# Kernel tuning notes

Measured on AMD Instinct MI355X. Metric: run time of the kernel, lower is better.

## Reference

```python
import jax, jax.numpy as jnp
import numpy as np

BS = 32  # leaf block size


def setup_inputs() -> dict:
    key = jax.random.key(0)
    ks = jax.random.split(key, 10)
    N, C, E, H = 262144, 128, 4194304, 4
    x = jax.random.normal(ks[0], (1, N, C), jnp.float32)
    rows = jax.random.randint(ks[1], (E,), 0, N, dtype=jnp.int32)
    offs = jax.random.randint(ks[2], (E,), -16, 16, dtype=jnp.int32)
    cols = jnp.clip(rows + offs, 0, N - 1)
    edge_index = jnp.stack([rows, cols], axis=0)  # (2, E) int32
    edge_values = jax.random.normal(ks[3], (E,), jnp.float32)
    positions = jax.random.uniform(ks[4], (N, 3), jnp.float32)
    qkv_w = jax.random.normal(ks[5], (C, 3 * C), jnp.float32) * 0.02
    qkv_b = jnp.zeros((3 * C,), jnp.float32)
    proj_w = jax.random.normal(ks[6], (C, C), jnp.float32) * 0.02
    proj_b = jnp.zeros((C,), jnp.float32)
    gate_w = jax.random.normal(ks[7], (H, 1), jnp.float32) * 0.01  # nn.Linear(1, H)
    gate_b = jnp.zeros((H,), jnp.float32)
    return {"x": x, "edge_index": edge_index, "edge_values": edge_values,
            "positions": positions, "qkv_w": qkv_w, "qkv_b": qkv_b,
            "proj_w": proj_w, "proj_b": proj_b, "gate_w": gate_w, "gate_b": gate_b}


def _build_leaf_block_connectivity(edge_index, edge_values, positions, num_blocks, dtype):
    # Returns attn_mask (nb, 32, 33) and edge_feats (nb, 32, 33, 4) = (dx,dy,dz,w).
    rows, cols = edge_index[0], edge_index[1]
    br, bc = rows // BS, cols // BS
    in_blk = (br == bc) & (br < num_blocks)
    b_safe = jnp.where(in_blk, br, num_blocks)  # out-of-block edges -> dummy block
    rl, cl = rows % BS, cols % BS
    dx = positions[cols] - positions[rows]               # (E, 3)
    ef_flat = jnp.concatenate([dx, edge_values[:, None]], axis=1).astype(dtype)  # (E, 4)
    diag = jnp.arange(BS)
    attn_mask = jnp.zeros((num_blocks + 1, BS, BS + 1), dtype)
    attn_mask = attn_mask.at[:, diag, diag].set(1.0)      # self
    attn_mask = attn_mask.at[:, :, BS].set(1.0)           # block node
    attn_mask = attn_mask.at[b_safe, rl, cl].set(1.0)     # edges
    edge_feats = jnp.zeros((num_blocks + 1, BS, BS + 1, 4), dtype)
    edge_feats = edge_feats.at[b_safe, rl, cl].set(ef_flat)
    return attn_mask[:num_blocks], edge_feats[:num_blocks]


def reference(x, edge_index, edge_values, positions, qkv_w, qkv_b, proj_w, proj_b, gate_w, gate_b):
    B, N, C = x.shape
    H = gate_b.shape[0]
    hd = C // H
    scale = hd ** -0.5
    nb = N // BS
    dtype = x.dtype
    attn_mask, edge_feats = _build_leaf_block_connectivity(edge_index, edge_values, positions, nb, dtype)

    x_blk = x.reshape(B, nb, BS, C)
    block_node = x_blk.mean(axis=2, keepdims=True)            # (B, nb, 1, C)
    kv = jnp.concatenate([x_blk, block_node], axis=2)          # (B, nb, 33, C)
    qkv_q = x_blk @ qkv_w + qkv_b
    qkv_kv = kv @ qkv_w + qkv_b
    q = qkv_q[..., :C].reshape(B, nb, BS, H, hd)
    k = qkv_kv[..., C:2 * C].reshape(B, nb, BS + 1, H, hd)
    v = qkv_kv[..., 2 * C:].reshape(B, nb, BS + 1, H, hd)

    scores = jnp.einsum('bnqhd,bnkhd->bnqkh', q, k) * scale    # (B, nb, 32, 33, H)

    diag = jnp.arange(BS)
    w_bias = edge_feats[..., 3]                                # (nb, 32, 33)
    w_bias = w_bias.at[:, :, BS].set(1.0)
    w_bias = w_bias.at[:, diag, diag].set(1.0)
    scores = scores + w_bias[None, :, :, :, None]

    mask = attn_mask[None, :, :, :, None]                      # (1, nb, 32, 33, 1)
    neg = jnp.asarray(-1e9, dtype)
    scores = jnp.where(mask == 0, neg, scores)
    attn_probs = jax.nn.softmax(scores, axis=3)

    # edge_gate: Linear(1, H) applied to w_bias, zeroed where masked, added post-softmax
    gate = w_bias[..., None] * gate_w[:, 0] + gate_b           # (nb, 32, 33, H)
    gate = jnp.where(mask[0] == 0, 0.0, gate)[None]            # (1, nb, 32, 33, H)
    combined = attn_probs + gate

    out = jnp.einsum('bnqkh,bnkhd->bnqhd', combined, v).reshape(B, N, C)
    return out @ proj_w + proj_b
```

## Files before the change

kernel.cpp:

```cpp
#include <hip/hip_runtime.h>
#include <hip/hip_bf16.h>

#define BS 32
#define NBC 33

typedef unsigned long long ull;
typedef __attribute__((ext_vector_type(8))) __bf16 bf16x8;
typedef __attribute__((ext_vector_type(4))) float f32x4;
typedef __attribute__((ext_vector_type(4))) unsigned short us4;

__device__ __forceinline__ unsigned short f2b(float f) {
    __hip_bfloat16 h = __float2bfloat16(f);
    return *reinterpret_cast<unsigned short*>(&h);
}
__device__ __forceinline__ float b2f(unsigned short u) {
    union { unsigned int i; float f; } x; x.i = ((unsigned int)u) << 16; return x.f;
}
#define LD8(p) (*reinterpret_cast<const bf16x8*>(p))

#define ZB 2048
__global__ void zero_prepack_kernel(uint4* __restrict__ tbl4, int n4,
                                    const float* __restrict__ qkv_w,
                                    const float* __restrict__ proj_w,
                                    unsigned short* __restrict__ wq,
                                    unsigned short* __restrict__ wp) {
    if (blockIdx.x < ZB) {
        int stride = ZB * 256;
        for (int i = blockIdx.x * 256 + threadIdx.x; i < n4; i += stride)
            tbl4[i] = make_uint4(0u, 0u, 0u, 0u);
    } else {
        int tid = (blockIdx.x - ZB) * 256 + threadIdx.x;
        int f = tid >> 9, lane = (tid >> 3) & 63, j = tid & 7;
        int ks = f & 3;
        int kk = ks * 32 + (lane >> 4) * 8 + j;
        int nn = lane & 15;
        if (f < 96) {
            int t = f >> 2;
            int w = t / 6, s = t % 6;
            int g = (s < 2) ? (2 * w + s) : (s < 4) ? (8 + 2 * w + (s - 2)) : (16 + 2 * w + (s - 4));
            wq[tid] = f2b(qkv_w[kk * 384 + g * 16 + nn]);
        } else {
            int f2 = f - 96;
            wp[f2 * 512 + lane * 8 + j] = f2b(proj_w[kk * 128 + (f2 >> 2) * 16 + nn]);
        }
    }
}

__global__ void edge_scatter_kernel(const int* __restrict__ rows,
                                    const int* __restrict__ cols,
                                    unsigned* __restrict__ tbl, int E) {
    int base = (blockIdx.x * 256 + threadIdx.x) * 4;
    if (base >= E) return;
    if (base + 4 <= E) {
        int4 r4 = *reinterpret_cast<const int4*>(rows + base);
        int4 c4 = *reinterpret_cast<const int4*>(cols + base);
        int rr[4] = {r4.x, r4.y, r4.z, r4.w};
        int cc[4] = {c4.x, c4.y, c4.z, c4.w};
        #pragma unroll
        for (int k = 0; k < 4; ++k) {
            int r = rr[k], c = cc[k];
            if ((r >> 5) == (c >> 5) && r != c)
                atomicMax(&tbl[((size_t)(r >> 5) * BS + (r & 31)) * NBC + (c & 31)],
                          (unsigned)(base + k + 1));
        }
    } else {
        for (int e = base; e < E && e < base + 4; ++e) {
            int r = rows[e], c = cols[e];
            if ((r >> 5) == (c >> 5) && r != c)
                atomicMax(&tbl[((size_t)(r >> 5) * BS + (r & 31)) * NBC + (c & 31)],
                          (unsigned)(e + 1));
        }
    }
}

__global__ __launch_bounds__(256)
void block_attn_kernel(const float* __restrict__ x,
                       const unsigned* __restrict__ tbl,
                       const float* __restrict__ vals,
                       const unsigned short* __restrict__ wq,
                       const unsigned short* __restrict__ wp,
                       const float* __restrict__ qkv_b,
                       const float* __restrict__ proj_b,
                       const float* __restrict__ gate_w,
                       const float* __restrict__ gate_b,
                       float* __restrict__ out) {
    __shared__ __align__(16) unsigned short xs[32][136];
    __shared__ __align__(16) unsigned short qs[4][32][40];
    __shared__ __align__(16) unsigned short ksm[4][34][40];
    __shared__ __align__(16) unsigned short vT[4][32][40];
    __shared__ float pcol[4][32];

    const int b = blockIdx.x, t = threadIdx.x;
    const int w = t >> 6, l = t & 63, g16 = l >> 4, c16 = l & 15;
    const f32x4 z4 = {0.f, 0.f, 0.f, 0.f};
    const float NEG = -1.0e30f;

    const float* xb = x + (size_t)b * (BS * 128);
    #pragma unroll
    for (int it = 0; it < 4; ++it) {
        int idx = (t + it * 256) * 4;
        float4 v = *reinterpret_cast<const float4*>(xb + idx);
        us4 u; u.x = f2b(v.x); u.y = f2b(v.y); u.z = f2b(v.z); u.w = f2b(v.w);
        *reinterpret_cast<us4*>(&xs[idx >> 7][idx & 127]) = u;
    }
    if (l < 32) ksm[w][33][l] = 0;

    float wb[2][4][3];
    {
        const unsigned* tb = tbl + (size_t)b * (BS * NBC);
        unsigned idr[2][4][2];
        #pragma unroll
        for (int mt = 0; mt < 2; ++mt)
            #pragma unroll
            for (int r = 0; r < 4; ++r) {
                const int i = 16 * mt + 4 * g16 + r;
                #pragma unroll
                for (int nt = 0; nt < 2; ++nt)
                    idr[mt][r][nt] = tb[i * NBC + 16 * nt + c16];
            }
        #pragma unroll
        for (int mt = 0; mt < 2; ++mt)
            #pragma unroll
            for (int r = 0; r < 4; ++r) {
                const int i = 16 * mt + 4 * g16 + r;
                #pragma unroll
                for (int nt = 0; nt < 2; ++nt) {
                    const int j = 16 * nt + c16;
                    const unsigned id = idr[mt][r][nt];
                    wb[mt][r][nt] = (j == i) ? 1.f : (id ? vals[id - 1] : NEG);
                }
                wb[mt][r][2] = (c16 == 0) ? 1.f : NEG;
            }
    }
    __syncthreads();

    bf16x8 a[2][4];
    #pragma unroll
    for (int mt = 0; mt < 2; ++mt)
        #pragma unroll
        for (int ks = 0; ks < 4; ++ks)
            a[mt][ks] = LD8(&xs[c16 + 16 * mt][ks * 32 + g16 * 8]);

    {
        const unsigned short* wqs = wq + (size_t)(w * 24) * 512 + l * 8;
        #pragma unroll
        for (int s = 0; s < 6; ++s) {
            bf16x8 bn[4];
            #pragma unroll
            for (int ks = 0; ks < 4; ++ks) bn[ks] = LD8(wqs + (s * 4 + ks) * 512);
            f32x4 acc0 = z4, acc1 = z4;
            #pragma unroll
            for (int ks = 0; ks < 4; ++ks) {
                acc0 = __builtin_amdgcn_mfma_f32_16x16x32_bf16(a[0][ks], bn[ks], acc0, 0, 0, 0);
                acc1 = __builtin_amdgcn_mfma_f32_16x16x32_bf16(a[1][ks], bn[ks], acc1, 0, 0, 0);
            }
            const float bias = qkv_b[(s >> 1) * 128 + 32 * w + 16 * (s & 1) + c16];
            const int cc = 16 * (s & 1) + c16;
            if (s < 2) {
                #pragma unroll
                for (int r = 0; r < 4; ++r) {
                    qs[w][4 * g16 + r][cc]      = f2b(acc0[r] + bias);
                    qs[w][16 + 4 * g16 + r][cc] = f2b(acc1[r] + bias);
                }
            } else {
                float csum = acc0[0] + acc0[1] + acc0[2] + acc0[3]
                           + acc1[0] + acc1[1] + acc1[2] + acc1[3];
                csum += __shfl_xor(csum, 16, 64);
                csum += __shfl_xor(csum, 32, 64);
                const float meanv = csum * (1.f / 32.f) + bias;
                if (s < 4) {
                    #pragma unroll
                    for (int r = 0; r < 4; ++r) {
                        ksm[w][4 * g16 + r][cc]      = f2b(acc0[r] + bias);
                        ksm[w][16 + 4 * g16 + r][cc] = f2b(acc1[r] + bias);
                    }
                    if (g16 == 0) ksm[w][32][cc] = f2b(meanv);
                } else {
                    #pragma unroll
                    for (int r = 0; r < 4; ++r) {
                        vT[w][cc][4 * g16 + r]      = f2b(acc0[r] + bias);
                        vT[w][cc][16 + 4 * g16 + r] = f2b(acc1[r] + bias);
                    }
                    if (g16 == 0) vT[w][cc][32] = f2b(meanv);
                }
            }
        }
    }
    __syncthreads();

    f32x4 s[2][3];
    {
        bf16x8 aq0 = LD8(&qs[w][c16][g16 * 8]);
        bf16x8 aq1 = LD8(&qs[w][16 + c16][g16 * 8]);
        bf16x8 bk0 = LD8(&ksm[w][c16][g16 * 8]);
        bf16x8 bk1 = LD8(&ksm[w][16 + c16][g16 * 8]);
        const int n2 = (c16 == 0) ? 32 : 33;
        bf16x8 bk2 = LD8(&ksm[w][n2][g16 * 8]);
        s[0][0] = __builtin_amdgcn_mfma_f32_16x16x32_bf16(aq0, bk0, z4, 0, 0, 0);
        s[0][1] = __builtin_amdgcn_mfma_f32_16x16x32_bf16(aq0, bk1, z4, 0, 0, 0);
        s[0][2] = __builtin_amdgcn_mfma_f32_16x16x32_bf16(aq0, bk2, z4, 0, 0, 0);
        s[1][0] = __builtin_amdgcn_mfma_f32_16x16x32_bf16(aq1, bk0, z4, 0, 0, 0);
        s[1][1] = __builtin_amdgcn_mfma_f32_16x16x32_bf16(aq1, bk1, z4, 0, 0, 0);
        s[1][2] = __builtin_amdgcn_mfma_f32_16x16x32_bf16(aq1, bk2, z4, 0, 0, 0);
    }

    {
        const float scale = 0.17677669529663687f;
        const float gwh = gate_w[w], gbh = gate_b[w];
        #pragma unroll
        for (int mt = 0; mt < 2; ++mt)
            #pragma unroll
            for (int r = 0; r < 4; ++r) {
                const int i = 16 * mt + 4 * g16 + r;
                float sc[3];
                #pragma unroll
                for (int k = 0; k < 3; ++k) sc[k] = s[mt][k][r] * scale + wb[mt][r][k];
                float mx = fmaxf(fmaxf(sc[0], sc[1]), sc[2]);
                mx = fmaxf(mx, __shfl_xor(mx, 1, 64));
                mx = fmaxf(mx, __shfl_xor(mx, 2, 64));
                mx = fmaxf(mx, __shfl_xor(mx, 4, 64));
                mx = fmaxf(mx, __shfl_xor(mx, 8, 64));
                float e0 = __expf(sc[0] - mx), e1 = __expf(sc[1] - mx), e2 = __expf(sc[2] - mx);
                float sum = e0 + e1 + e2;
                sum += __shfl_xor(sum, 1, 64);
                sum += __shfl_xor(sum, 2, 64);
                sum += __shfl_xor(sum, 4, 64);
                sum += __shfl_xor(sum, 8, 64);
                const float inv = __builtin_amdgcn_rcpf(sum);
                float gt0 = (wb[mt][r][0] > -1.0e29f) ? wb[mt][r][0] * gwh + gbh : 0.f;
                float gt1 = (wb[mt][r][1] > -1.0e29f) ? wb[mt][r][1] * gwh + gbh : 0.f;
                float gt2 = (wb[mt][r][2] > -1.0e29f) ? gwh + gbh : 0.f;
                qs[w][i][c16]      = f2b(e0 * inv + gt0);
                qs[w][i][16 + c16] = f2b(e1 * inv + gt1);
                if (c16 == 0) pcol[w][i] = e2 * inv + gt2;
            }
    }
    __syncthreads();

    {
        bf16x8 ap0 = LD8(&qs[w][c16][g16 * 8]);
        bf16x8 ap1 = LD8(&qs[w][16 + c16][g16 * 8]);
        f32x4 o[2][2];
        #pragma unroll
        for (int nt = 0; nt < 2; ++nt) {
            bf16x8 bv = LD8(&vT[w][16 * nt + c16][g16 * 8]);
            o[0][nt] = __builtin_amdgcn_mfma_f32_16x16x32_bf16(ap0, bv, z4, 0, 0, 0);
            o[1][nt] = __builtin_amdgcn_mfma_f32_16x16x32_bf16(ap1, bv, z4, 0, 0, 0);
        }
        #pragma unroll
        for (int nt = 0; nt < 2; ++nt) {
            const float vm = b2f(vT[w][16 * nt + c16][32]);
            #pragma unroll
            for (int mt = 0; mt < 2; ++mt)
                #pragma unroll
                for (int r = 0; r < 4; ++r)
                    o[mt][nt][r] += pcol[w][16 * mt + 4 * g16 + r] * vm;
        }
        #pragma unroll
        for (int mt = 0; mt < 2; ++mt)
            #pragma unroll
            for (int nt = 0; nt < 2; ++nt)
                #pragma unroll
                for (int r = 0; r < 4; ++r)
                    qs[w][16 * mt + 4 * g16 + r][16 * nt + c16] = f2b(o[mt][nt][r]);
    }
    __syncthreads();

    {
        bf16x8 aa[2][4];
        #pragma unroll
        for (int mt = 0; mt < 2; ++mt)
            #pragma unroll
            for (int h = 0; h < 4; ++h)
                aa[mt][h] = LD8(&qs[h][c16 + 16 * mt][g16 * 8]);
        f32x4 po[2][2];
        po[0][0] = z4; po[0][1] = z4; po[1][0] = z4; po[1][1] = z4;
        const unsigned short* wps = wp + l * 8;
        #pragma unroll
        for (int nt = 0; nt < 2; ++nt)
            #pragma unroll
            for (int h = 0; h < 4; ++h) {
                bf16x8 bw = LD8(wps + (size_t)((2 * w + nt) * 4 + h) * 512);
                po[0][nt] = __builtin_amdgcn_mfma_f32_16x16x32_bf16(aa[0][h], bw, po[0][nt], 0, 0, 0);
                po[1][nt] = __builtin_amdgcn_mfma_f32_16x16x32_bf16(aa[1][h], bw, po[1][nt], 0, 0, 0);
            }
        float* ob = out + (size_t)b * (BS * 128);
        #pragma unroll
        for (int nt = 0; nt < 2; ++nt) {
            const int col = 32 * w + 16 * nt + c16;
            const float pbv = proj_b[col];
            #pragma unroll
            for (int mt = 0; mt < 2; ++mt)
                #pragma unroll
                for (int r = 0; r < 4; ++r)
                    ob[(size_t)(16 * mt + 4 * g16 + r) * 128 + col] = po[mt][nt][r] + pbv;
        }
    }
}

extern "C" void kernel_launch(void* const* d_in, const int* in_sizes, int n_in,
                              void* d_out, int out_size, void* d_ws, size_t ws_size,
                              hipStream_t stream) {
    const float* x      = (const float*)d_in[0];
    const int*   ei     = (const int*)d_in[1];
    const float* ev     = (const float*)d_in[2];
    const float* qkv_w  = (const float*)d_in[4];
    const float* qkv_b  = (const float*)d_in[5];
    const float* proj_w = (const float*)d_in[6];
    const float* proj_b = (const float*)d_in[7];
    const float* gate_w = (const float*)d_in[8];
    const float* gate_b = (const float*)d_in[9];
    float* out = (float*)d_out;

    const int E  = in_sizes[2];
    const int N  = in_sizes[0] / 128;
    const int nb = N / BS;

    unsigned* tbl = (unsigned*)d_ws;
    size_t twords = (size_t)nb * BS * NBC;
    size_t tbytes = (twords * sizeof(unsigned) + 255) & ~(size_t)255;
    unsigned short* wqp = (unsigned short*)((char*)d_ws + tbytes);
    unsigned short* wpp = wqp + 96 * 512;

    zero_prepack_kernel<<<ZB + 256, 256, 0, stream>>>((uint4*)tbl, (int)(twords / 4),
                                                      qkv_w, proj_w, wqp, wpp);
    edge_scatter_kernel<<<((E + 3) / 4 + 255) / 256, 256, 0, stream>>>(ei, ei + E, tbl, E);
    block_attn_kernel<<<nb, 256, 0, stream>>>(x, tbl, ev, wqp, wpp, qkv_b, proj_b,
                                              gate_w, gate_b, out);
}
```

Before: 270.8 us.

## Pack edge id and value into 64-bit atomic key, alias shared memory

The edge scatter now does a 64-bit atomicMax on a key holding the edge index in the high word and the edge value bits in the low word. The attention kernel can then read the weight straight from the table instead of making a dependent random gather into vals. Shared memory is merged into one buffer with xs aliased over vT, plus an extra barrier, to lower LDS use and allow more resident blocks. In exchange the table doubles in size, so zeroing and reading it costs more bandwidth, and 64-bit atomics may be slower.

```diff
diff --git a/kernel.cpp b/kernel.cpp
--- a/kernel.cpp
+++ b/kernel.cpp
@@ -48,35 +48,39 @@
 
 __global__ void edge_scatter_kernel(const int* __restrict__ rows,
                                     const int* __restrict__ cols,
-                                    unsigned* __restrict__ tbl, int E) {
+                                    const float* __restrict__ vals,
+                                    ull* __restrict__ tbl, int E) {
     int base = (blockIdx.x * 256 + threadIdx.x) * 4;
     if (base >= E) return;
     if (base + 4 <= E) {
         int4 r4 = *reinterpret_cast<const int4*>(rows + base);
         int4 c4 = *reinterpret_cast<const int4*>(cols + base);
+        float4 v4 = *reinterpret_cast<const float4*>(vals + base);
         int rr[4] = {r4.x, r4.y, r4.z, r4.w};
         int cc[4] = {c4.x, c4.y, c4.z, c4.w};
+        float vv[4] = {v4.x, v4.y, v4.z, v4.w};
         #pragma unroll
         for (int k = 0; k < 4; ++k) {
             int r = rr[k], c = cc[k];
-            if ((r >> 5) == (c >> 5) && r != c)
-                atomicMax(&tbl[((size_t)(r >> 5) * BS + (r & 31)) * NBC + (c & 31)],
-                          (unsigned)(base + k + 1));
+            if ((r >> 5) == (c >> 5) && r != c) {
+                ull key = ((ull)(unsigned)(base + k + 1) << 32) | (ull)__float_as_uint(vv[k]);
+                atomicMax(&tbl[((size_t)(r >> 5) * BS + (r & 31)) * NBC + (c & 31)], key);
+            }
         }
     } else {
         for (int e = base; e < E && e < base + 4; ++e) {
             int r = rows[e], c = cols[e];
-            if ((r >> 5) == (c >> 5) && r != c)
-                atomicMax(&tbl[((size_t)(r >> 5) * BS + (r & 31)) * NBC + (c & 31)],
-                          (unsigned)(e + 1));
+            if ((r >> 5) == (c >> 5) && r != c) {
+                ull key = ((ull)(unsigned)(e + 1) << 32) | (ull)__float_as_uint(vals[e]);
+                atomicMax(&tbl[((size_t)(r >> 5) * BS + (r & 31)) * NBC + (c & 31)], key);
+            }
         }
     }
 }
 
 __global__ __launch_bounds__(256)
 void block_attn_kernel(const float* __restrict__ x,
-                       const unsigned* __restrict__ tbl,
-                       const float* __restrict__ vals,
+                       const ull* __restrict__ tbl,
                        const unsigned short* __restrict__ wq,
                        const unsigned short* __restrict__ wp,
                        const float* __restrict__ qkv_b,
@@ -84,11 +88,12 @@
                        const float* __restrict__ gate_w,
                        const float* __restrict__ gate_b,
                        float* __restrict__ out) {
-    __shared__ __align__(16) unsigned short xs[32][136];
-    __shared__ __align__(16) unsigned short qs[4][32][40];
-    __shared__ __align__(16) unsigned short ksm[4][34][40];
-    __shared__ __align__(16) unsigned short vT[4][32][40];
-    __shared__ float pcol[4][32];
+    __shared__ __align__(16) unsigned char smem[31872];
+    unsigned short (*qs)[32][40]  = (unsigned short (*)[32][40])(smem);
+    unsigned short (*ksm)[34][40] = (unsigned short (*)[34][40])(smem + 10240);
+    unsigned short (*vT)[32][40]  = (unsigned short (*)[32][40])(smem + 21120);
+    float (*pcol)[32]             = (float (*)[32])(smem + 31360);
+    unsigned short (*xs)[136]     = (unsigned short (*)[136])(smem + 21120);
 
     const int b = blockIdx.x, t = threadIdx.x;
     const int w = t >> 6, l = t & 63, g16 = l >> 4, c16 = l & 15;
@@ -107,27 +112,18 @@
 
     float wb[2][4][3];
     {
-        const unsigned* tb = tbl + (size_t)b * (BS * NBC);
-        unsigned idr[2][4][2];
+        const ull* tb = tbl + (size_t)b * (BS * NBC);
         #pragma unroll
         for (int mt = 0; mt < 2; ++mt)
             #pragma unroll
             for (int r = 0; r < 4; ++r) {
                 const int i = 16 * mt + 4 * g16 + r;
                 #pragma unroll
-                for (int nt = 0; nt < 2; ++nt)
-                    idr[mt][r][nt] = tb[i * NBC + 16 * nt + c16];
-            }
-        #pragma unroll
-        for (int mt = 0; mt < 2; ++mt)
-            #pragma unroll
-            for (int r = 0; r < 4; ++r) {
-                const int i = 16 * mt + 4 * g16 + r;
-                #pragma unroll
                 for (int nt = 0; nt < 2; ++nt) {
                     const int j = 16 * nt + c16;
-                    const unsigned id = idr[mt][r][nt];
-                    wb[mt][r][nt] = (j == i) ? 1.f : (id ? vals[id - 1] : NEG);
+                    const ull wv = tb[i * NBC + j];
+                    wb[mt][r][nt] = (j == i) ? 1.f
+                                   : (wv ? __uint_as_float((unsigned)(wv & 0xffffffffu)) : NEG);
                 }
                 wb[mt][r][2] = (c16 == 0) ? 1.f : NEG;
             }
@@ -140,6 +136,7 @@
         #pragma unroll
         for (int ks = 0; ks < 4; ++ks)
             a[mt][ks] = LD8(&xs[c16 + 16 * mt][ks * 32 + g16 * 8]);
+    __syncthreads();
 
     {
         const unsigned short* wqs = wq + (size_t)(w * 24) * 512 + l * 8;
@@ -316,15 +313,16 @@
     const int N  = in_sizes[0] / 128;
     const int nb = N / BS;
 
-    unsigned* tbl = (unsigned*)d_ws;
+    ull* tbl = (ull*)d_ws;
     size_t twords = (size_t)nb * BS * NBC;
-    size_t tbytes = (twords * sizeof(unsigned) + 255) & ~(size_t)255;
+    size_t tbytes = (twords * sizeof(ull) + 255) & ~(size_t)255;
     unsigned short* wqp = (unsigned short*)((char*)d_ws + tbytes);
     unsigned short* wpp = wqp + 96 * 512;
 
-    zero_prepack_kernel<<<ZB + 256, 256, 0, stream>>>((uint4*)tbl, (int)(twords / 4),
+    zero_prepack_kernel<<<ZB + 256, 256, 0, stream>>>((uint4*)tbl,
+                                                      (int)(twords * sizeof(ull) / 16),
                                                       qkv_w, proj_w, wqp, wpp);
-    edge_scatter_kernel<<<((E + 3) / 4 + 255) / 256, 256, 0, stream>>>(ei, ei + E, tbl, E);
-    block_attn_kernel<<<nb, 256, 0, stream>>>(x, tbl, ev, wqp, wpp, qkv_b, proj_b,
+    edge_scatter_kernel<<<((E + 3) / 4 + 255) / 256, 256, 0, stream>>>(ei, ei + E, ev, tbl, E);
+    block_attn_kernel<<<nb, 256, 0, stream>>>(x, tbl, wqp, wpp, qkv_b, proj_b,
                                               gate_w, gate_b, out);
 }
```

Measured after the change: 259.1 us. 1.05x faster.
